# Kernel optimization log

Hardware: AMD Instinct MI355X
Metric: run time of the kernel (lower is better)

Reference implementation:

```python
import jax, jax.numpy as jnp
import numpy as np

B, C, H, W = 8, 256, 64, 64

def setup_inputs() -> dict:
    key = jax.random.key(0)
    ks = jax.random.split(key, 8)
    s = 0.05  # keep 1x1-conv outputs well-scaled
    return {
        "x": jax.random.normal(ks[0], (B, C, H, W), jnp.float32),
        "Wq": jax.random.normal(ks[1], (C, C), jnp.float32) * s,
        "bq": jax.random.normal(ks[2], (C,), jnp.float32) * s,
        "Wk": jax.random.normal(ks[3], (C, C), jnp.float32) * s,
        "bk": jax.random.normal(ks[4], (C,), jnp.float32) * s,
        "Wv": jax.random.normal(ks[5], (C, C), jnp.float32) * s,
        "bv": jax.random.normal(ks[6], (C,), jnp.float32) * s,
        "gamma": jax.random.normal(ks[7], (1,), jnp.float32),
    }

def reference(x, Wq, bq, Wk, bk, Wv, bv, gamma):
    bs, ch, w, h = x.shape
    n = w * h
    xf = x.reshape(bs, ch, n)                                  # (B, C, N)
    # 1x1 convs == per-position channel matmuls
    q = jnp.einsum('oc,bcn->bon', Wq, xf) + bq[None, :, None]  # (B, C, N)
    k = jnp.einsum('oc,bcn->bon', Wk, xf) + bk[None, :, None]
    v = jnp.einsum('oc,bcn->bon', Wv, xf) + bv[None, :, None]
    # energy[b,i,j] = <q[:,i], k[:,j]>
    energy = jnp.einsum('bci,bcj->bij', q, k)                  # (B, N, N)
    # NOTE: unusual post-softmax scaling by 1/sqrt(N), as in the source
    attn = jax.nn.softmax(energy, axis=-1) / jnp.sqrt(jnp.asarray(n, x.dtype))
    # out[b,c,i] = sum_j v[b,c,j] * attn[b,i,j]
    out = jnp.einsum('bcj,bij->bci', v, attn).reshape(bs, ch, w, h)
    return gamma[0] * out + x
```

## Files before the change

### kernel.cpp

```cpp
#include <hip/hip_runtime.h>

#define B_ 8
#define C_ 256
#define N_ 4096

typedef __attribute__((ext_vector_type(8))) __bf16 bf16x8;
typedef __attribute__((ext_vector_type(4))) float f32x4;

__device__ __forceinline__ unsigned short f2bf(float f) {
  union { float f; unsigned u; } v; v.f = f;
  unsigned r = v.u + 0x7fffu + ((v.u >> 16) & 1u);
  return (unsigned short)(r >> 16);
}

__device__ __forceinline__ uint4 pack8(const float* s) {
  uint4 o;
  o.x = (unsigned)f2bf(s[0]) | ((unsigned)f2bf(s[1]) << 16);
  o.y = (unsigned)f2bf(s[2]) | ((unsigned)f2bf(s[3]) << 16);
  o.z = (unsigned)f2bf(s[4]) | ((unsigned)f2bf(s[5]) << 16);
  o.w = (unsigned)f2bf(s[6]) | ((unsigned)f2bf(s[7]) << 16);
  return o;
}

__device__ __forceinline__ void dma16(const void* g, void* l) {
  __builtin_amdgcn_global_load_lds(
      (const __attribute__((address_space(1))) unsigned int*)(uintptr_t)g,
      (__attribute__((address_space(3))) unsigned int*)(uintptr_t)l, 16, 0, 0);
}

__global__ __launch_bounds__(256) void prep(
    const float* __restrict__ x,
    const float* __restrict__ Wq, const float* __restrict__ Wk,
    const float* __restrict__ Wv,
    unsigned short* __restrict__ xT, unsigned short* __restrict__ Wbf)
{
  __shared__ unsigned int xTl[64][33];
  const int t   = threadIdx.x;
  const int n0  = blockIdx.x * 64;
  const int ct0 = blockIdx.y * 64;
  const int b   = blockIdx.z;

  if (blockIdx.z == 0) {
    const int bid = blockIdx.x + 64 * blockIdx.y;
    if (bid < 96) {
      const int el0 = (bid * 256 + t) * 8;
      const int mat = el0 >> 16;
      const int off = el0 & 65535;
      const float* src = (mat == 0) ? Wq : (mat == 1) ? Wk : Wv;
      float tmp[8];
      float4 f0 = ((const float4*)(src + off))[0];
      float4 f1 = ((const float4*)(src + off))[1];
      tmp[0]=f0.x; tmp[1]=f0.y; tmp[2]=f0.z; tmp[3]=f0.w;
      tmp[4]=f1.x; tmp[5]=f1.y; tmp[6]=f1.z; tmp[7]=f1.w;
      *(uint4*)(Wbf + el0) = pack8(tmp);
    }
  }

  {
    const int cp = t >> 3;
    const int nq = t & 7;
    const float* s0 = x + ((size_t)(b * C_ + ct0 + 2*cp) * N_ + n0 + nq * 8);
    const float* s1 = s0 + N_;
    float4 a0 = ((const float4*)s0)[0], a1 = ((const float4*)s0)[1];
    float4 b0 = ((const float4*)s1)[0], b1 = ((const float4*)s1)[1];
    float lo[8] = {a0.x,a0.y,a0.z,a0.w,a1.x,a1.y,a1.z,a1.w};
    float hi[8] = {b0.x,b0.y,b0.z,b0.w,b1.x,b1.y,b1.z,b1.w};
    #pragma unroll
    for (int k = 0; k < 8; ++k)
      xTl[nq*8 + k][cp] = (unsigned)f2bf(lo[k]) | ((unsigned)f2bf(hi[k]) << 16);
  }
  __syncthreads();

  {
    const int n = t >> 2, cq = t & 3;
    unsigned int vals[8];
    #pragma unroll
    for (int g = 0; g < 8; ++g) vals[g] = xTl[n][cq*8 + g];
    uint4* dst = (uint4*)(xT + ((size_t)(b * N_ + n0 + n)) * C_ + ct0 + cq*16);
    dst[0] = make_uint4(vals[0], vals[1], vals[2], vals[3]);
    dst[1] = make_uint4(vals[4], vals[5], vals[6], vals[7]);
  }
}

__global__ __launch_bounds__(256, 2) void qkv_gemm(
    const unsigned short* __restrict__ xT, const unsigned short* __restrict__ Wbf,
    const float* __restrict__ bq, const float* __restrict__ bk,
    const float* __restrict__ bv,
    unsigned short* __restrict__ qT, unsigned short* __restrict__ kT,
    unsigned short* __restrict__ vW)
{
  __shared__ char smraw[49152];

  const int t    = threadIdx.x;
  const int lane = t & 63;
  const int w    = t >> 6;
  const int m16  = lane & 15;
  const int q    = (lane >> 4) & 3;
  const int nt0  = blockIdx.x * 128;
  const int b    = blockIdx.y;
  const int mat  = blockIdx.z;
  const size_t bN = (size_t)b * N_;

  const unsigned short* Wm = Wbf + mat * 65536;
  const float* bm = (mat == 0) ? bq : (mat == 1) ? bk : bv;
  unsigned short* outp = (mat == 0) ? qT : (mat == 1) ? kT : vW;

  auto stage = [&](int buf, int cs) {
    #pragma unroll
    for (int p = 0; p < 4; ++p) {
      const int row = 64 * w + 16 * p + (lane >> 2);
      const int g   = (lane & 3) ^ (row & 3);
      dma16(Wm + row * 256 + cs * 32 + g * 8,
            smraw + buf * 16384 + (64 * w + 16 * p) * 64);
    }
    #pragma unroll
    for (int p = 0; p < 2; ++p) {
      const int row = 32 * w + 16 * p + (lane >> 2);
      const int g   = (lane & 3) ^ (row & 3);
      dma16(xT + (bN + nt0 + row) * 256 + cs * 32 + g * 8,
            smraw + 32768 + buf * 8192 + (32 * w + 16 * p) * 64);
    }
  };

  stage(0, 0);

  float br[4][4];
  #pragma unroll
  for (int ob = 0; ob < 4; ++ob)
    #pragma unroll
    for (int r = 0; r < 4; ++r) br[ob][r] = bm[64*w + ob*16 + q*4 + r];

  f32x4 acc[4][8] = {};

  for (int cs = 0; cs < 8; ++cs) {
    asm volatile("s_waitcnt vmcnt(0)" ::: "memory");
    __syncthreads();
    if (cs + 1 < 8) stage((cs + 1) & 1, cs + 1);
    const int buf = cs & 1;
    const unsigned short* Wt = (const unsigned short*)(smraw + buf * 16384);
    const unsigned short* Xt = (const unsigned short*)(smraw + 32768 + buf * 8192);

    bf16x8 af[4], bf_[8];
    #pragma unroll
    for (int ob = 0; ob < 4; ++ob) {
      const int o = 64*w + ob*16 + m16;
      af[ob] = *(const bf16x8*)&Wt[o * 32 + ((q ^ (o & 3)) * 8)];
    }
    #pragma unroll
    for (int nb = 0; nb < 8; ++nb) {
      const int n = nb*16 + m16;
      bf_[nb] = *(const bf16x8*)&Xt[n * 32 + ((q ^ (n & 3)) * 8)];
    }
    #pragma unroll
    for (int ob = 0; ob < 4; ++ob)
      #pragma unroll
      for (int nb = 0; nb < 8; ++nb)
        acc[ob][nb] = __builtin_amdgcn_mfma_f32_16x16x32_bf16(af[ob], bf_[nb], acc[ob][nb], 0,0,0);
  }

  float* Dst = (float*)smraw;
  for (int nc = 0; nc < 4; ++nc) {
    __syncthreads();
    #pragma unroll
    for (int ob = 0; ob < 4; ++ob)
      #pragma unroll
      for (int h = 0; h < 2; ++h) {
        const int nb = nc*2 + h;
        #pragma unroll
        for (int r = 0; r < 4; ++r)
          Dst[(64*w + ob*16 + q*4 + r) * 36 + h*16 + m16] = acc[ob][nb][r] + br[ob][r];
      }
    __syncthreads();

    if (mat < 2) {
      const int n_loc = t & 31, oc = t >> 5;
      float vals[32];
      #pragma unroll
      for (int k = 0; k < 32; ++k) vals[k] = Dst[(oc*32 + k) * 36 + n_loc];
      uint4* dst = (uint4*)(outp + (bN + nt0 + nc*32 + n_loc) * C_ + oc*32);
      #pragma unroll
      for (int g = 0; g < 4; ++g) dst[g] = pack8(vals + g*8);
    } else {
      float vals[32], pv[32];
      #pragma unroll
      for (int k = 0; k < 32; ++k) vals[k] = Dst[t * 36 + k];
      #pragma unroll
      for (int p = 0; p < 32; ++p)
        pv[p] = vals[16*((p>>2)&1) + 4*(p>>3) + (p&3)];
      uint4* dst = (uint4*)(outp + ((size_t)(b * C_ + t)) * N_ + nt0 + nc*32);
      #pragma unroll
      for (int g = 0; g < 4; ++g) dst[g] = pack8(pv + g*8);
    }
  }
}

__global__ __launch_bounds__(256, 2) void attn9(
    const unsigned short* __restrict__ qT, const unsigned short* __restrict__ kT,
    const unsigned short* __restrict__ vW,
    float* __restrict__ Op0, float* __restrict__ Op1,
    float* __restrict__ l0p, float* __restrict__ l1p)
{
  __shared__ unsigned short Kbuf[2][32 * 256];
  __shared__ unsigned short Vbuf[3][256 * 32];

  const int t    = threadIdx.x;
  const int lane = t & 63;
  const int w    = t >> 6;
  const int b    = blockIdx.x;
  const int i0   = blockIdx.y * 128;
  const int jh   = blockIdx.z;
  const int jbase = jh * 2048;
  const int m16  = lane & 15;
  const int q    = (lane >> 4) & 3;
  const int q8   = q * 8;
  const size_t bN = (size_t)b * N_;
  const size_t bC = (size_t)b * C_;

  auto stageK = [&](int buf, int j0) {
    #pragma unroll
    for (int p = 0; p < 4; ++p) {
      const int row = 8*w + 2*p + (lane >> 5);
      const int g   = (lane & 31) ^ (row & 7);
      dma16(kT + (bN + j0 + row) * C_ + g * 8, &Kbuf[buf][(8*w + 2*p) * 256]);
    }
  };
  auto stageV = [&](int buf, int j0) {
    #pragma unroll
    for (int p = 0; p < 4; ++p) {
      const int row = 64*w + 16*p + (lane >> 2);
      const int g   = (lane & 3) ^ ((row >> 1) & 3);
      dma16(vW + (bC + row) * N_ + j0 + g * 8, &Vbuf[buf][(64*w + 16*p) * 32]);
    }
  };

  stageK(0, jbase); stageV(0, jbase);

  bf16x8 qfA[8], qfB[8];
  {
    const unsigned short* qa = qT + ((bN + i0 + w*32 + m16) * C_ + q8);
    const unsigned short* qb = qa + 16 * C_;
    #pragma unroll
    for (int ks = 0; ks < 8; ++ks) {
      qfA[ks] = *(const bf16x8*)(qa + ks*32);
      qfB[ks] = *(const bf16x8*)(qb + ks*32);
    }
  }

  float lA = 0.0f, lB = 0.0f;
  f32x4 OA[16] = {}, OB[16] = {};
  uint4 pkA, pkB;
  int vb_prev = 0;

  {
    asm volatile("s_waitcnt vmcnt(0)" ::: "memory");
    __syncthreads();
    stageK(1, jbase + 32); stageV(1, jbase + 32);
    const unsigned short* Kt = Kbuf[0];

    f32x4 sA[2] = {}, sB[2] = {};
    __builtin_amdgcn_s_setprio(1);
    #pragma unroll
    for (int ks = 0; ks < 8; ++ks)
      #pragma unroll
      for (int jb = 0; jb < 2; ++jb) {
        const int j = jb*16 + m16;
        bf16x8 a = *(const bf16x8*)&Kt[j * 256 + (((4*ks + q) ^ (j & 7)) * 8)];
        sA[jb] = __builtin_amdgcn_mfma_f32_16x16x32_bf16(a, qfA[ks], sA[jb], 0,0,0);
        sB[jb] = __builtin_amdgcn_mfma_f32_16x16x32_bf16(a, qfB[ks], sB[jb], 0,0,0);
      }
    __builtin_amdgcn_s_setprio(0);

    float psA[2][4], psB[2][4];
    #pragma unroll
    for (int jb = 0; jb < 2; ++jb)
      #pragma unroll
      for (int r = 0; r < 4; ++r) {
        const float pa = __expf(sA[jb][r] - 64.0f);
        const float pb = __expf(sB[jb][r] - 64.0f);
        psA[jb][r] = pa; lA += pa;
        psB[jb][r] = pb; lB += pb;
      }
    pkA.x = (unsigned)f2bf(psA[0][0]) | ((unsigned)f2bf(psA[0][1]) << 16);
    pkA.y = (unsigned)f2bf(psA[0][2]) | ((unsigned)f2bf(psA[0][3]) << 16);
    pkA.z = (unsigned)f2bf(psA[1][0]) | ((unsigned)f2bf(psA[1][1]) << 16);
    pkA.w = (unsigned)f2bf(psA[1][2]) | ((unsigned)f2bf(psA[1][3]) << 16);
    pkB.x = (unsigned)f2bf(psB[0][0]) | ((unsigned)f2bf(psB[0][1]) << 16);
    pkB.y = (unsigned)f2bf(psB[0][2]) | ((unsigned)f2bf(psB[0][3]) << 16);
    pkB.z = (unsigned)f2bf(psB[1][0]) | ((unsigned)f2bf(psB[1][1]) << 16);
    pkB.w = (unsigned)f2bf(psB[1][2]) | ((unsigned)f2bf(psB[1][3]) << 16);
  }

  for (int jt = 1; jt < 64; ++jt) {
    asm volatile("s_waitcnt vmcnt(0)" ::: "memory");
    __syncthreads();
    const int vb_cur = (vb_prev == 2) ? 0 : vb_prev + 1;
    const int vb_nxt = (vb_cur == 2) ? 0 : vb_cur + 1;
    if (jt + 1 < 64) { stageK((jt + 1) & 1, jbase + (jt + 1) * 32); stageV(vb_nxt, jbase + (jt + 1) * 32); }

    const unsigned short* Kt = Kbuf[jt & 1];
    const unsigned short* Vp = Vbuf[vb_prev];
    union { uint4 u; bf16x8 v; } pva; pva.u = pkA;
    union { uint4 u; bf16x8 v; } pvb; pvb.u = pkB;

    f32x4 sA[2] = {}, sB[2] = {};
    __builtin_amdgcn_s_setprio(1);
    #pragma unroll
    for (int u = 0; u < 16; ++u) {
      {
        const int ks = u >> 1, jb = u & 1;
        const int j = jb*16 + m16;
        bf16x8 a = *(const bf16x8*)&Kt[j * 256 + (((4*ks + q) ^ (j & 7)) * 8)];
        sA[jb] = __builtin_amdgcn_mfma_f32_16x16x32_bf16(a, qfA[ks], sA[jb], 0,0,0);
        sB[jb] = __builtin_amdgcn_mfma_f32_16x16x32_bf16(a, qfB[ks], sB[jb], 0,0,0);
      }
      {
        const int c = u*16 + m16;
        bf16x8 vf = *(const bf16x8*)&Vp[c * 32 + ((q ^ ((c >> 1) & 3)) * 8)];
        OA[u] = __builtin_amdgcn_mfma_f32_16x16x32_bf16(vf, pva.v, OA[u], 0,0,0);
        OB[u] = __builtin_amdgcn_mfma_f32_16x16x32_bf16(vf, pvb.v, OB[u], 0,0,0);
      }
    }
    __builtin_amdgcn_s_setprio(0);

    float psA[2][4], psB[2][4];
    #pragma unroll
    for (int jb = 0; jb < 2; ++jb)
      #pragma unroll
      for (int r = 0; r < 4; ++r) {
        const float pa = __expf(sA[jb][r] - 64.0f);
        const float pb = __expf(sB[jb][r] - 64.0f);
        psA[jb][r] = pa; lA += pa;
        psB[jb][r] = pb; lB += pb;
      }
    pkA.x = (unsigned)f2bf(psA[0][0]) | ((unsigned)f2bf(psA[0][1]) << 16);
    pkA.y = (unsigned)f2bf(psA[0][2]) | ((unsigned)f2bf(psA[0][3]) << 16);
    pkA.z = (unsigned)f2bf(psA[1][0]) | ((unsigned)f2bf(psA[1][1]) << 16);
    pkA.w = (unsigned)f2bf(psA[1][2]) | ((unsigned)f2bf(psA[1][3]) << 16);
    pkB.x = (unsigned)f2bf(psB[0][0]) | ((unsigned)f2bf(psB[0][1]) << 16);
    pkB.y = (unsigned)f2bf(psB[0][2]) | ((unsigned)f2bf(psB[0][3]) << 16);
    pkB.z = (unsigned)f2bf(psB[1][0]) | ((unsigned)f2bf(psB[1][1]) << 16);
    pkB.w = (unsigned)f2bf(psB[1][2]) | ((unsigned)f2bf(psB[1][3]) << 16);
    vb_prev = vb_cur;
  }

  {
    const unsigned short* Vp = Vbuf[vb_prev];
    union { uint4 u; bf16x8 v; } pva; pva.u = pkA;
    union { uint4 u; bf16x8 v; } pvb; pvb.u = pkB;
    __builtin_amdgcn_s_setprio(1);
    #pragma unroll
    for (int cb = 0; cb < 16; ++cb) {
      const int c = cb*16 + m16;
      bf16x8 vf = *(const bf16x8*)&Vp[c * 32 + ((q ^ ((c >> 1) & 3)) * 8)];
      OA[cb] = __builtin_amdgcn_mfma_f32_16x16x32_bf16(vf, pva.v, OA[cb], 0,0,0);
      OB[cb] = __builtin_amdgcn_mfma_f32_16x16x32_bf16(vf, pvb.v, OB[cb], 0,0,0);
    }
    __builtin_amdgcn_s_setprio(0);
  }

  float lAs = lA;
  lAs += __shfl_xor(lAs, 16);
  lAs += __shfl_xor(lAs, 32);
  float lBs = lB;
  lBs += __shfl_xor(lBs, 16);
  lBs += __shfl_xor(lBs, 32);

  float* Op = (jh == 0) ? Op0 : Op1;
  float* lp = ((jh == 0) ? l0p : l1p) + (size_t)b * N_;
  const int icolA = i0 + w*32 + m16;
  if (lane < 16) { lp[icolA] = lAs; lp[icolA + 16] = lBs; }
  #pragma unroll
  for (int cb = 0; cb < 16; ++cb) {
    #pragma unroll
    for (int r = 0; r < 4; ++r) {
      const int c = cb*16 + q*4 + r;
      const size_t idx = (bC + c) * N_ + icolA;
      Op[idx] = OA[cb][r];
      Op[idx + 16] = OB[cb][r];
    }
  }
}

__global__ __launch_bounds__(256) void combine(
    const float* __restrict__ Op1, const float* __restrict__ l0p,
    const float* __restrict__ l1p, const float* __restrict__ x,
    const float* __restrict__ gamma, float* __restrict__ out)
{
  const int idx4 = blockIdx.x * 256 + threadIdx.x;
  const int i4   = idx4 & 1023;
  const int b    = idx4 >> 18;
  const float gm = gamma[0];

  float4 o0 = ((const float4*)out)[idx4];
  float4 o1 = ((const float4*)Op1)[idx4];
  float4 xv = ((const float4*)x)[idx4];
  float4 la = ((const float4*)(l0p + (size_t)b * N_))[i4];
  float4 lb = ((const float4*)(l1p + (size_t)b * N_))[i4];

  float4 r;
  r.x = (o0.x + o1.x) * (gm / ((la.x + lb.x) * 64.0f)) + xv.x;
  r.y = (o0.y + o1.y) * (gm / ((la.y + lb.y) * 64.0f)) + xv.y;
  r.z = (o0.z + o1.z) * (gm / ((la.z + lb.z) * 64.0f)) + xv.z;
  r.w = (o0.w + o1.w) * (gm / ((la.w + lb.w) * 64.0f)) + xv.w;
  ((float4*)out)[idx4] = r;
}

extern "C" void kernel_launch(void* const* d_in, const int* in_sizes, int n_in,
                              void* d_out, int out_size, void* d_ws, size_t ws_size,
                              hipStream_t stream) {
  const float* x     = (const float*)d_in[0];
  const float* Wq    = (const float*)d_in[1];
  const float* bq    = (const float*)d_in[2];
  const float* Wk    = (const float*)d_in[3];
  const float* bk    = (const float*)d_in[4];
  const float* Wv    = (const float*)d_in[5];
  const float* bv    = (const float*)d_in[6];
  const float* gamma = (const float*)d_in[7];
  float* out = (float*)d_out;

  unsigned short* xT  = (unsigned short*)d_ws;
  unsigned short* Wbf = xT + (size_t)B_ * N_ * C_;
  unsigned short* qT  = Wbf + 3 * 65536;
  unsigned short* kT  = qT + (size_t)B_ * N_ * C_;
  unsigned short* vW  = kT + (size_t)B_ * N_ * C_;
  float* Op1 = (float*)(vW + (size_t)B_ * N_ * C_);
  float* l0p = Op1 + (size_t)B_ * C_ * N_;
  float* l1p = l0p + (size_t)B_ * N_;

  prep<<<dim3(64, 4, 8), dim3(256), 0, stream>>>(x, Wq, Wk, Wv, xT, Wbf);
  qkv_gemm<<<dim3(32, 8, 3), dim3(256), 0, stream>>>(xT, Wbf, bq, bk, bv, qT, kT, vW);
  attn9<<<dim3(8, 32, 2), dim3(256), 0, stream>>>(qT, kT, vW, out, Op1, l0p, l1p);
  combine<<<dim3(8192), dim3(256), 0, stream>>>(Op1, l0p, l1p, x, gamma, out);
}
```

Measured before the change: 300.4 us.

## Switch attention kernel to 32x32x16 MFMA with lane-shuffled P fragments

Rewrites the attention inner loop to use 32x32x16 bf16 MFMAs instead of pairs of 16x16x32 MFMAs, which changes the fragment layout of Q, K, V and the output accumulators. The probability fragment for the PV product is built by exchanging packed bf16 halves across lane halves with a shuffle, and the packing uses the hardware v_cvt_pk_bf16_f32 instruction. The V column permutation in the qkv kernel is dropped to match the new layout, and the per-tile wait is loosened to vmcnt(4) so the next tile's loads can stay in flight. This aims to cut MFMA issue count and LDS reads per FLOP, at the cost of extra cross-lane shuffles, a different rounding path, and a riskier synchronization scheme.

```diff
diff --git a/kernel.cpp b/kernel.cpp
--- a/kernel.cpp
+++ b/kernel.cpp
@@ -6,6 +6,7 @@
 
 typedef __attribute__((ext_vector_type(8))) __bf16 bf16x8;
 typedef __attribute__((ext_vector_type(4))) float f32x4;
+typedef __attribute__((ext_vector_type(16))) float f32x16;
 
 __device__ __forceinline__ unsigned short f2bf(float f) {
   union { float f; unsigned u; } v; v.f = f;
@@ -181,20 +182,17 @@
       #pragma unroll
       for (int g = 0; g < 4; ++g) dst[g] = pack8(vals + g*8);
     } else {
-      float vals[32], pv[32];
+      float vals[32];
       #pragma unroll
       for (int k = 0; k < 32; ++k) vals[k] = Dst[t * 36 + k];
-      #pragma unroll
-      for (int p = 0; p < 32; ++p)
-        pv[p] = vals[16*((p>>2)&1) + 4*(p>>3) + (p&3)];
       uint4* dst = (uint4*)(outp + ((size_t)(b * C_ + t)) * N_ + nt0 + nc*32);
       #pragma unroll
-      for (int g = 0; g < 4; ++g) dst[g] = pack8(pv + g*8);
-    }
-  }
-}
-
-__global__ __launch_bounds__(256, 2) void attn9(
+      for (int g = 0; g < 4; ++g) dst[g] = pack8(vals + g*8);
+    }
+  }
+}
+
+__global__ __launch_bounds__(256, 2) void attn10(
     const unsigned short* __restrict__ qT, const unsigned short* __restrict__ kT,
     const unsigned short* __restrict__ vW,
     float* __restrict__ Op0, float* __restrict__ Op1,
@@ -206,13 +204,12 @@
   const int t    = threadIdx.x;
   const int lane = t & 63;
   const int w    = t >> 6;
+  const int il   = lane & 31;
+  const int hi   = lane >> 5;
   const int b    = blockIdx.x;
   const int i0   = blockIdx.y * 128;
   const int jh   = blockIdx.z;
   const int jbase = jh * 2048;
-  const int m16  = lane & 15;
-  const int q    = (lane >> 4) & 3;
-  const int q8   = q * 8;
   const size_t bN = (size_t)b * N_;
   const size_t bC = (size_t)b * C_;
 
@@ -235,148 +232,142 @@
 
   stageK(0, jbase); stageV(0, jbase);
 
-  bf16x8 qfA[8], qfB[8];
+  bf16x8 qf[16];
   {
-    const unsigned short* qa = qT + ((bN + i0 + w*32 + m16) * C_ + q8);
-    const unsigned short* qb = qa + 16 * C_;
-    #pragma unroll
-    for (int ks = 0; ks < 8; ++ks) {
-      qfA[ks] = *(const bf16x8*)(qa + ks*32);
-      qfB[ks] = *(const bf16x8*)(qb + ks*32);
-    }
-  }
-
-  float lA = 0.0f, lB = 0.0f;
-  f32x4 OA[16] = {}, OB[16] = {};
-  uint4 pkA, pkB;
+    const unsigned short* qbase = qT + (bN + i0 + w*32 + il) * C_ + hi*8;
+    #pragma unroll
+    for (int cs = 0; cs < 16; ++cs) qf[cs] = *(const bf16x8*)(qbase + cs*16);
+  }
+
+  const int kb  = il * 256;
+  const int kx8 = (il & 7) * 8;
+  const int sv  = (il >> 1) & 3;
+
+  float l_lane = 0.0f;
+  f32x16 Oacc[8] = {};
+  unsigned int wv[4][2], pv[4][2];
   int vb_prev = 0;
 
+  auto buildPF = [&](uint4& f0, uint4& f1) {
+    f0.x = hi ? pv[1][0] : wv[0][0];
+    f0.y = hi ? pv[1][1] : wv[0][1];
+    f0.z = hi ? wv[1][0] : pv[0][0];
+    f0.w = hi ? wv[1][1] : pv[0][1];
+    f1.x = hi ? pv[3][0] : wv[2][0];
+    f1.y = hi ? pv[3][1] : wv[2][1];
+    f1.z = hi ? wv[3][0] : pv[2][0];
+    f1.w = hi ? wv[3][1] : pv[2][1];
+  };
+
   {
-    asm volatile("s_waitcnt vmcnt(0)" ::: "memory");
+    asm volatile("s_waitcnt vmcnt(4)" ::: "memory");
     __syncthreads();
     stageK(1, jbase + 32); stageV(1, jbase + 32);
     const unsigned short* Kt = Kbuf[0];
 
-    f32x4 sA[2] = {}, sB[2] = {};
+    f32x16 st = {};
     __builtin_amdgcn_s_setprio(1);
     #pragma unroll
-    for (int ks = 0; ks < 8; ++ks)
-      #pragma unroll
-      for (int jb = 0; jb < 2; ++jb) {
-        const int j = jb*16 + m16;
-        bf16x8 a = *(const bf16x8*)&Kt[j * 256 + (((4*ks + q) ^ (j & 7)) * 8)];
-        sA[jb] = __builtin_amdgcn_mfma_f32_16x16x32_bf16(a, qfA[ks], sA[jb], 0,0,0);
-        sB[jb] = __builtin_amdgcn_mfma_f32_16x16x32_bf16(a, qfB[ks], sB[jb], 0,0,0);
-      }
+    for (int u = 0; u < 16; ++u) {
+      bf16x8 a = *(const bf16x8*)&Kt[kb + (((2*u + hi) * 8) ^ kx8)];
+      st = __builtin_amdgcn_mfma_f32_32x32x16_bf16(a, qf[u], st, 0, 0, 0);
+    }
     __builtin_amdgcn_s_setprio(0);
 
-    float psA[2][4], psB[2][4];
-    #pragma unroll
-    for (int jb = 0; jb < 2; ++jb)
-      #pragma unroll
-      for (int r = 0; r < 4; ++r) {
-        const float pa = __expf(sA[jb][r] - 64.0f);
-        const float pb = __expf(sB[jb][r] - 64.0f);
-        psA[jb][r] = pa; lA += pa;
-        psB[jb][r] = pb; lB += pb;
-      }
-    pkA.x = (unsigned)f2bf(psA[0][0]) | ((unsigned)f2bf(psA[0][1]) << 16);
-    pkA.y = (unsigned)f2bf(psA[0][2]) | ((unsigned)f2bf(psA[0][3]) << 16);
-    pkA.z = (unsigned)f2bf(psA[1][0]) | ((unsigned)f2bf(psA[1][1]) << 16);
-    pkA.w = (unsigned)f2bf(psA[1][2]) | ((unsigned)f2bf(psA[1][3]) << 16);
-    pkB.x = (unsigned)f2bf(psB[0][0]) | ((unsigned)f2bf(psB[0][1]) << 16);
-    pkB.y = (unsigned)f2bf(psB[0][2]) | ((unsigned)f2bf(psB[0][3]) << 16);
-    pkB.z = (unsigned)f2bf(psB[1][0]) | ((unsigned)f2bf(psB[1][1]) << 16);
-    pkB.w = (unsigned)f2bf(psB[1][2]) | ((unsigned)f2bf(psB[1][3]) << 16);
+    #pragma unroll
+    for (int g = 0; g < 4; ++g) {
+      float p0 = __expf(st[4*g+0] - 64.0f);
+      float p1 = __expf(st[4*g+1] - 64.0f);
+      float p2 = __expf(st[4*g+2] - 64.0f);
+      float p3 = __expf(st[4*g+3] - 64.0f);
+      l_lane += (p0 + p1) + (p2 + p3);
+      asm("v_cvt_pk_bf16_f32 %0, %1, %2" : "=v"(wv[g][0]) : "v"(p0), "v"(p1));
+      asm("v_cvt_pk_bf16_f32 %0, %1, %2" : "=v"(wv[g][1]) : "v"(p2), "v"(p3));
+    }
+    #pragma unroll
+    for (int g = 0; g < 4; ++g) {
+      pv[g][0] = __shfl_xor((int)wv[g][0], 32);
+      pv[g][1] = __shfl_xor((int)wv[g][1], 32);
+    }
   }
 
   for (int jt = 1; jt < 64; ++jt) {
-    asm volatile("s_waitcnt vmcnt(0)" ::: "memory");
+    asm volatile("s_waitcnt vmcnt(4)" ::: "memory");
     __syncthreads();
     const int vb_cur = (vb_prev == 2) ? 0 : vb_prev + 1;
     const int vb_nxt = (vb_cur == 2) ? 0 : vb_cur + 1;
-    if (jt + 1 < 64) { stageK((jt + 1) & 1, jbase + (jt + 1) * 32); stageV(vb_nxt, jbase + (jt + 1) * 32); }
+    if (jt + 1 < 64) { stageK((jt + 1) & 1, jbase + (jt + 1) * 32);
+                       stageV(vb_nxt, jbase + (jt + 1) * 32); }
 
     const unsigned short* Kt = Kbuf[jt & 1];
     const unsigned short* Vp = Vbuf[vb_prev];
-    union { uint4 u; bf16x8 v; } pva; pva.u = pkA;
-    union { uint4 u; bf16x8 v; } pvb; pvb.u = pkB;
-
-    f32x4 sA[2] = {}, sB[2] = {};
+    union { uint4 u; bf16x8 v; } pf0, pf1;
+    buildPF(pf0.u, pf1.u);
+
+    f32x16 st = {};
     __builtin_amdgcn_s_setprio(1);
     #pragma unroll
     for (int u = 0; u < 16; ++u) {
       {
-        const int ks = u >> 1, jb = u & 1;
-        const int j = jb*16 + m16;
-        bf16x8 a = *(const bf16x8*)&Kt[j * 256 + (((4*ks + q) ^ (j & 7)) * 8)];
-        sA[jb] = __builtin_amdgcn_mfma_f32_16x16x32_bf16(a, qfA[ks], sA[jb], 0,0,0);
-        sB[jb] = __builtin_amdgcn_mfma_f32_16x16x32_bf16(a, qfB[ks], sB[jb], 0,0,0);
+        bf16x8 a = *(const bf16x8*)&Kt[kb + (((2*u + hi) * 8) ^ kx8)];
+        st = __builtin_amdgcn_mfma_f32_32x32x16_bf16(a, qf[u], st, 0, 0, 0);
       }
       {
-        const int c = u*16 + m16;
-        bf16x8 vf = *(const bf16x8*)&Vp[c * 32 + ((q ^ ((c >> 1) & 3)) * 8)];
-        OA[u] = __builtin_amdgcn_mfma_f32_16x16x32_bf16(vf, pva.v, OA[u], 0,0,0);
-        OB[u] = __builtin_amdgcn_mfma_f32_16x16x32_bf16(vf, pvb.v, OB[u], 0,0,0);
+        const int ct = u & 7, js = u >> 3;
+        bf16x8 vf = *(const bf16x8*)&Vp[ct*1024 + il*32 + (((2*js + hi) ^ sv) * 8)];
+        Oacc[ct] = __builtin_amdgcn_mfma_f32_32x32x16_bf16(
+            vf, js ? pf1.v : pf0.v, Oacc[ct], 0, 0, 0);
       }
     }
     __builtin_amdgcn_s_setprio(0);
 
-    float psA[2][4], psB[2][4];
-    #pragma unroll
-    for (int jb = 0; jb < 2; ++jb)
-      #pragma unroll
-      for (int r = 0; r < 4; ++r) {
-        const float pa = __expf(sA[jb][r] - 64.0f);
-        const float pb = __expf(sB[jb][r] - 64.0f);
-        psA[jb][r] = pa; lA += pa;
-        psB[jb][r] = pb; lB += pb;
-      }
-    pkA.x = (unsigned)f2bf(psA[0][0]) | ((unsigned)f2bf(psA[0][1]) << 16);
-    pkA.y = (unsigned)f2bf(psA[0][2]) | ((unsigned)f2bf(psA[0][3]) << 16);
-    pkA.z = (unsigned)f2bf(psA[1][0]) | ((unsigned)f2bf(psA[1][1]) << 16);
-    pkA.w = (unsigned)f2bf(psA[1][2]) | ((unsigned)f2bf(psA[1][3]) << 16);
-    pkB.x = (unsigned)f2bf(psB[0][0]) | ((unsigned)f2bf(psB[0][1]) << 16);
-    pkB.y = (unsigned)f2bf(psB[0][2]) | ((unsigned)f2bf(psB[0][3]) << 16);
-    pkB.z = (unsigned)f2bf(psB[1][0]) | ((unsigned)f2bf(psB[1][1]) << 16);
-    pkB.w = (unsigned)f2bf(psB[1][2]) | ((unsigned)f2bf(psB[1][3]) << 16);
+    #pragma unroll
+    for (int g = 0; g < 4; ++g) {
+      float p0 = __expf(st[4*g+0] - 64.0f);
+      float p1 = __expf(st[4*g+1] - 64.0f);
+      float p2 = __expf(st[4*g+2] - 64.0f);
+      float p3 = __expf(st[4*g+3] - 64.0f);
+      l_lane += (p0 + p1) + (p2 + p3);
+      asm("v_cvt_pk_bf16_f32 %0, %1, %2" : "=v"(wv[g][0]) : "v"(p0), "v"(p1));
+      asm("v_cvt_pk_bf16_f32 %0, %1, %2" : "=v"(wv[g][1]) : "v"(p2), "v"(p3));
+    }
+    #pragma unroll
+    for (int g = 0; g < 4; ++g) {
+      pv[g][0] = __shfl_xor((int)wv[g][0], 32);
+      pv[g][1] = __shfl_xor((int)wv[g][1], 32);
+    }
     vb_prev = vb_cur;
   }
 
+  asm volatile("s_waitcnt vmcnt(0)" ::: "memory");
+  __syncthreads();
   {
     const unsigned short* Vp = Vbuf[vb_prev];
-    union { uint4 u; bf16x8 v; } pva; pva.u = pkA;
-    union { uint4 u; bf16x8 v; } pvb; pvb.u = pkB;
+    union { uint4 u; bf16x8 v; } pf0, pf1;
+    buildPF(pf0.u, pf1.u);
     __builtin_amdgcn_s_setprio(1);
     #pragma unroll
-    for (int cb = 0; cb < 16; ++cb) {
-      const int c = cb*16 + m16;
-      bf16x8 vf = *(const bf16x8*)&Vp[c * 32 + ((q ^ ((c >> 1) & 3)) * 8)];
-      OA[cb] = __builtin_amdgcn_mfma_f32_16x16x32_bf16(vf, pva.v, OA[cb], 0,0,0);
-      OB[cb] = __builtin_amdgcn_mfma_f32_16x16x32_bf16(vf, pvb.v, OB[cb], 0,0,0);
+    for (int u = 0; u < 16; ++u) {
+      const int ct = u & 7, js = u >> 3;
+      bf16x8 vf = *(const bf16x8*)&Vp[ct*1024 + il*32 + (((2*js + hi) ^ sv) * 8)];
+      Oacc[ct] = __builtin_amdgcn_mfma_f32_32x32x16_bf16(
+          vf, js ? pf1.v : pf0.v, Oacc[ct], 0, 0, 0);
     }
     __builtin_amdgcn_s_setprio(0);
   }
 
-  float lAs = lA;
-  lAs += __shfl_xor(lAs, 16);
-  lAs += __shfl_xor(lAs, 32);
-  float lBs = lB;
-  lBs += __shfl_xor(lBs, 16);
-  lBs += __shfl_xor(lBs, 32);
+  const float ls = l_lane + __shfl_xor(l_lane, 32);
 
   float* Op = (jh == 0) ? Op0 : Op1;
   float* lp = ((jh == 0) ? l0p : l1p) + (size_t)b * N_;
-  const int icolA = i0 + w*32 + m16;
-  if (lane < 16) { lp[icolA] = lAs; lp[icolA + 16] = lBs; }
+  const int icol = i0 + w*32 + il;
+  if (hi == 0) lp[icol] = ls;
   #pragma unroll
-  for (int cb = 0; cb < 16; ++cb) {
-    #pragma unroll
-    for (int r = 0; r < 4; ++r) {
-      const int c = cb*16 + q*4 + r;
-      const size_t idx = (bC + c) * N_ + icolA;
-      Op[idx] = OA[cb][r];
-      Op[idx + 16] = OB[cb][r];
+  for (int ct = 0; ct < 8; ++ct) {
+    #pragma unroll
+    for (int r = 0; r < 16; ++r) {
+      const int c = ct*32 + (r & 3) + 8*(r >> 2) + 4*hi;
+      Op[(bC + c) * N_ + icol] = Oacc[ct][r];
     }
   }
 }
@@ -429,6 +420,6 @@
 
   prep<<<dim3(64, 4, 8), dim3(256), 0, stream>>>(x, Wq, Wk, Wv, xT, Wbf);
   qkv_gemm<<<dim3(32, 8, 3), dim3(256), 0, stream>>>(xT, Wbf, bq, bk, bv, qT, kT, vW);
-  attn9<<<dim3(8, 32, 2), dim3(256), 0, stream>>>(qT, kT, vW, out, Op1, l0p, l1p);
+  attn10<<<dim3(8, 32, 2), dim3(256), 0, stream>>>(qT, kT, vW, out, Op1, l0p, l1p);
   combine<<<dim3(8192), dim3(256), 0, stream>>>(Op1, l0p, l1p, x, gamma, out);
 }
```

Result: slower. 306.5 us (+2.0%).
